# Kernel optimization log

Measured on AMD Instinct MI355X. Metric: run time of the kernel, lower is better.

## Reference

```python
import jax, jax.numpy as jnp
import numpy as np

NUM_LAYERS = 3
INPUT_SIZE = 64
EMB = 128
NUM_CAT = 128          # must equal EMB for the W_e_proj assignment to shape-check
NUM_QUERIES = 1
INIT_SCALE = 0.02
KERNEL_PARAM = 1.0     # referenced-but-undefined in source; standard alpha=1
B = 16
N = 2048
D = INPUT_SIZE + 2 * EMB                 # 320, transformer embedding dim
F_IN = INPUT_SIZE + NUM_CAT + EMB        # 320, raw input feature dim


def setup_inputs() -> dict:
    key = jax.random.key(0)
    k = jax.random.split(key, 6)
    x = jax.random.normal(k[0], (B, F_IN, N), dtype=jnp.float32)
    embedding_matrix = jax.random.normal(k[1], (EMB, NUM_CAT), dtype=jnp.float32)
    W_Q = jax.random.normal(k[2], (NUM_LAYERS, 1, D, D), dtype=jnp.float32) * INIT_SCALE
    W_K = jax.random.normal(k[3], (NUM_LAYERS, 1, D, D), dtype=jnp.float32) * INIT_SCALE
    W_V = jax.random.normal(k[4], (NUM_LAYERS, 1, D, D), dtype=jnp.float32) * INIT_SCALE
    P = jax.random.normal(k[5], (NUM_LAYERS, 1, D, D), dtype=jnp.float32) * INIT_SCALE
    return {"x": x, "embedding_matrix": embedding_matrix,
            "W_Q": W_Q, "W_K": W_K, "W_V": W_V, "P": P}


def _build_We(embedding_matrix):
    W = jnp.zeros((D, F_IN), dtype=embedding_matrix.dtype)
    W = W.at[:INPUT_SIZE, :INPUT_SIZE].set(jnp.eye(INPUT_SIZE, dtype=W.dtype))
    W = W.at[D - EMB:, F_IN - EMB:].set(jnp.eye(EMB, dtype=W.dtype))
    # rows [input_size : D-emb], cols [input_size : F-num_categories]
    W = W.at[INPUT_SIZE:D - EMB, INPUT_SIZE:F_IN - NUM_CAT].set(embedding_matrix)
    return W


def reference(x, embedding_matrix, W_Q, W_K, W_V, P):
    W = _build_We(embedding_matrix)
    h = jnp.einsum('df,bfn->bdn', W, x)                        # [B, D, N]
    for nl in range(NUM_LAYERS):
        key = h[:, :, :-NUM_QUERIES]                           # include_query=False
        value = key
        query = h
        n_context = key.shape[-1]
        Q = jnp.einsum('id,bdm->bim', W_Q[nl, 0], query)       # [B, D, N]
        K = jnp.einsum('id,bdn->bin', W_K[nl, 0], key)         # [B, D, M]
        V = jnp.einsum('id,bdn->bin', W_V[nl, 0], value)       # [B, D, M]
        # linear kernel scores
        scores = KERNEL_PARAM * jnp.einsum('bim,bin->bmn', Q, K)  # [B, N, M]
        attn = jnp.einsum('bin,bmn->bim', V, scores) / n_context  # [B, D, N]
        h = h + jnp.einsum('ji,bim->bjm', P[nl, 0], attn)
    f = h[:, -EMB:, :]                                         # [B, EMB, N] (squeeze no-op for B>1)
    logits = jnp.einsum('bdn,dc->bnc', f, embedding_matrix)    # [B, N, C]
    predictions = jax.nn.softmax(logits, axis=-1)
    return logits, predictions
```

## Files before the change

kernel.cpp:

```cpp
#include <hip/hip_runtime.h>
#include <math.h>

typedef long long ll;
typedef unsigned int uint;
typedef unsigned short ushort;
typedef __attribute__((ext_vector_type(4))) float f32x4;
typedef __attribute__((ext_vector_type(8))) short bf16x8;

#define SZ 102400LL
#define RS 40960LL

__device__ inline void split2(float v, ushort& h, ushort& l)
{
    uint u = __float_as_uint(v);
    uint uh = u + (0x7FFFu + ((u >> 16) & 1u));
    h = (ushort)(uh >> 16);
    float hf = __uint_as_float((uint)h << 16);
    float d = v - hf;
    uint ud = __float_as_uint(d);
    l = (ushort)((ud + (0x7FFFu + ((ud >> 16) & 1u))) >> 16);
}
__device__ inline float us2f(ushort h, ushort l)
{
    return __uint_as_float((uint)h << 16) + __uint_as_float((uint)l << 16);
}

__global__ __launch_bounds__(256) void gram_sp_k(
    const float* __restrict__ x, float* __restrict__ part,
    const float* __restrict__ Wq, const float* __restrict__ Wk,
    const float* __restrict__ Wv, const float* __restrict__ P,
    const float* __restrict__ emb,
    ushort* __restrict__ WqTs, ushort* __restrict__ WkTs, ushort* __restrict__ WvTs,
    ushort* __restrict__ Ps, ushort* __restrict__ embs, ushort* __restrict__ embTs,
    float* __restrict__ q0)
{
    __shared__ __align__(16) char smem[20480];
    int bid0 = blockIdx.x, tid = threadIdx.x;
    if (bid0 < 960) {
        ushort* Ah  = (ushort*)smem;
        ushort* Al_ = Ah + 2560;
        ushort* Bh  = Al_ + 2560;
        ushort* Bl_ = Bh + 2560;
        int flat = bid0;
        int swz = (flat & 7) * 120 + (flat >> 3);
        int b = swz / 60;
        int rr = swz - b * 60;
        int p = rr / 15, t = rr - p * 15;
        int ti = 0, rem = t;
        while (rem >= 5 - ti) { rem -= 5 - ti; ++ti; }
        int tj = ti + rem;
        int i0 = ti * 64, j0 = tj * 64;
        bool diag = (ti == tj);
        const float* X = x + (ll)b * 320 * 2048;
        int wv = tid >> 6, lane = tid & 63;
        int lr = lane & 15, kb = (lane >> 4) * 8;
        int cr = tid >> 2, ck = (tid & 3) * 8;
        f32x4 hh[4], hl[4], lh[4];
        f32x4 zz = {0.f, 0.f, 0.f, 0.f};
        #pragma unroll
        for (int f = 0; f < 4; ++f) { hh[f] = zz; hl[f] = zz; lh[f] = zz; }
        const ushort* BhS = diag ? Ah : Bh;
        const ushort* BlS = diag ? Al_ : Bl_;

        for (int it = 0; it < 16; ++it) {
            int kg0 = p * 512 + it * 32;
            {
                const float* src = X + (ll)(i0 + cr) * 2048 + kg0 + ck;
                float4 v0 = *(const float4*)src;
                float4 v1 = *(const float4*)(src + 4);
                float vals[8] = {v0.x,v0.y,v0.z,v0.w,v1.x,v1.y,v1.z,v1.w};
                if (kg0 + ck + 7 >= 2047) {
                    #pragma unroll
                    for (int u = 0; u < 8; ++u) if (kg0 + ck + u >= 2047) vals[u] = 0.f;
                }
                bf16x8 hv, lv;
                #pragma unroll
                for (int u = 0; u < 8; ++u) { ushort h, l; split2(vals[u], h, l);
                                              hv[u] = (short)h; lv[u] = (short)l; }
                *(bf16x8*)&Ah[cr * 40 + ck] = hv;
                *(bf16x8*)&Al_[cr * 40 + ck] = lv;
            }
            if (!diag) {
                const float* src = X + (ll)(j0 + cr) * 2048 + kg0 + ck;
                float4 v0 = *(const float4*)src;
                float4 v1 = *(const float4*)(src + 4);
                float vals[8] = {v0.x,v0.y,v0.z,v0.w,v1.x,v1.y,v1.z,v1.w};
                if (kg0 + ck + 7 >= 2047) {
                    #pragma unroll
                    for (int u = 0; u < 8; ++u) if (kg0 + ck + u >= 2047) vals[u] = 0.f;
                }
                bf16x8 hv, lv;
                #pragma unroll
                for (int u = 0; u < 8; ++u) { ushort h, l; split2(vals[u], h, l);
                                              hv[u] = (short)h; lv[u] = (short)l; }
                *(bf16x8*)&Bh[cr * 40 + ck] = hv;
                *(bf16x8*)&Bl_[cr * 40 + ck] = lv;
            }
            __syncthreads();
            bf16x8 ah = *(const bf16x8*)&Ah[(wv * 16 + lr) * 40 + kb];
            bf16x8 al = *(const bf16x8*)&Al_[(wv * 16 + lr) * 40 + kb];
            #pragma unroll
            for (int f = 0; f < 4; ++f) {
                bf16x8 bh_ = *(const bf16x8*)&BhS[(f * 16 + lr) * 40 + kb];
                bf16x8 bl_ = *(const bf16x8*)&BlS[(f * 16 + lr) * 40 + kb];
                hh[f] = __builtin_amdgcn_mfma_f32_16x16x32_bf16(ah, bh_, hh[f], 0, 0, 0);
                hl[f] = __builtin_amdgcn_mfma_f32_16x16x32_bf16(ah, bl_, hl[f], 0, 0, 0);
                lh[f] = __builtin_amdgcn_mfma_f32_16x16x32_bf16(al, bh_, lh[f], 0, 0, 0);
            }
            __syncthreads();
        }
        float* out = part + (((ll)p * 16 + b) * 15 + t) * 4096;
        int orow0 = wv * 16 + (lane >> 4) * 4;
        #pragma unroll
        for (int f = 0; f < 4; ++f) {
            int col = f * 16 + lr;
            #pragma unroll
            for (int r = 0; r < 4; ++r)
                out[(orow0 + r) * 64 + col] = hh[f][r] + hl[f][r] + lh[f][r];
        }
        return;
    }
    int bid = bid0 - 960;
    float (*T)[65] = (float(*)[65])smem;
    if (bid < 225) {
        int m = bid / 25, t = bid % 25;
        const float* mats[3] = {Wq, Wk, Wv};
        ushort* dsts[3] = {WqTs, WkTs, WvTs};
        const float* src = mats[m / 3] + (ll)(m % 3) * SZ;
        ushort* dst = dsts[m / 3] + (ll)(m % 3) * SZ;
        int r0 = (t / 5) * 64, c0 = (t % 5) * 64;
        #pragma unroll
        for (int s = 0; s < 4; ++s) {
            int idx = s * 256 + tid;
            int r = idx >> 4, cq = (idx & 15) * 4;
            *(float4*)&T[r][cq] = *(const float4*)(src + (ll)(r0 + r) * 320 + c0 + cq);
        }
        __syncthreads();
        {
            int c = tid >> 2, kq = (tid & 3) * 16;
            bf16x8 h0, h1, l0, l1;
            #pragma unroll
            for (int u = 0; u < 8; ++u) {
                ushort h, l;
                split2(T[kq + u][c], h, l);     h0[u] = (short)h; l0[u] = (short)l;
                split2(T[kq + 8 + u][c], h, l); h1[u] = (short)h; l1[u] = (short)l;
            }
            ushort* dh = dst + (ll)(c0 + c) * 320 + r0 + kq;
            *(bf16x8*)dh = h0; *(bf16x8*)(dh + 8) = h1;
            *(bf16x8*)(dh + 3 * SZ) = l0; *(bf16x8*)(dh + 3 * SZ + 8) = l1;
        }
    } else if (bid < 375) {
        ll off = (ll)(bid - 225) * 2048 + tid * 8;
        float4 v0 = *(const float4*)(P + off);
        float4 v1 = *(const float4*)(P + off + 4);
        float vals[8] = {v0.x,v0.y,v0.z,v0.w,v1.x,v1.y,v1.z,v1.w};
        bf16x8 hv, lv;
        #pragma unroll
        for (int u = 0; u < 8; ++u) { ushort h,l; split2(vals[u],h,l);
                                      hv[u]=(short)h; lv[u]=(short)l; }
        *(bf16x8*)(Ps + off) = hv;
        *(bf16x8*)(Ps + off + 3 * SZ) = lv;
    } else if (bid < 383) {
        ll off = (ll)(bid - 375) * 2048 + tid * 8;
        float4 v0 = *(const float4*)(emb + off);
        float4 v1 = *(const float4*)(emb + off + 4);
        float vals[8] = {v0.x,v0.y,v0.z,v0.w,v1.x,v1.y,v1.z,v1.w};
        bf16x8 hv, lv;
        #pragma unroll
        for (int u = 0; u < 8; ++u) { ushort h,l; split2(vals[u],h,l);
                                      hv[u]=(short)h; lv[u]=(short)l; }
        *(bf16x8*)(embs + off) = hv;
        *(bf16x8*)(embs + off + 16384) = lv;
    } else if (bid < 387) {
        int t = bid - 383;
        int r0 = (t >> 1) * 64, c0 = (t & 1) * 64;
        {
            int r = tid >> 2, cq = (tid & 3) * 4;
            *(float4*)&T[r][cq]      = *(const float4*)(emb + (ll)(r0 + r) * 128 + c0 + cq);
            *(float4*)&T[r][cq + 16] = *(const float4*)(emb + (ll)(r0 + r) * 128 + c0 + cq + 16);
            *(float4*)&T[r][cq + 32] = *(const float4*)(emb + (ll)(r0 + r) * 128 + c0 + cq + 32);
            *(float4*)&T[r][cq + 48] = *(const float4*)(emb + (ll)(r0 + r) * 128 + c0 + cq + 48);
        }
        __syncthreads();
        {
            int c = tid >> 2, kq = (tid & 3) * 16;
            bf16x8 h0, h1, l0, l1;
            #pragma unroll
            for (int u = 0; u < 8; ++u) {
                ushort h, l;
                split2(T[kq + u][c], h, l);     h0[u]=(short)h; l0[u]=(short)l;
                split2(T[kq + 8 + u][c], h, l); h1[u]=(short)h; l1[u]=(short)l;
            }
            ushort* dh = embTs + (ll)(c0 + c) * 128 + r0 + kq;
            *(bf16x8*)dh = h0; *(bf16x8*)(dh + 8) = h1;
            *(bf16x8*)(dh + 16384) = l0; *(bf16x8*)(dh + 16384 + 8) = l1;
        }
    } else {
        ll base = (ll)(bid - 387) * 2048;
        #pragma unroll
        for (int s = 0; s < 8; ++s) {
            ll id = base + s * 256 + tid;
            int c = (int)(id / 320), i = (int)(id % 320);
            q0[id] = (i >= 192) ? emb[(ll)(i - 192) * 128 + c] : 0.f;
        }
    }
}

__global__ __launch_bounds__(256) void gram_red_k(const float* __restrict__ part,
                                                  ushort* __restrict__ GxS,
                                                  ushort* __restrict__ T1s)
{
    int bt = blockIdx.x;
    int b = bt / 15, t = bt % 15;
    int ti = 0, rem = t;
    while (rem >= 5 - ti) { rem -= 5 - ti; ++ti; }
    int tj = ti + rem;
    int i0 = ti * 64, j0 = tj * 64;
    int tid = threadIdx.x;
    int tx = tid & 15, rg = tid >> 4;
    bool wi = (ti == 0 || ti >= 3);
    bool wj = (tj == 0 || tj >= 3);
    ushort* Gb = GxS + (ll)b * SZ;
    ushort* Tsb = T1s + (ll)b * SZ;
    #pragma unroll
    for (int m = 0; m < 4; ++m) {
        int r = rg * 4 + m;
        float s[4] = {};
        for (int p = 0; p < 4; ++p) {
            const float* src = part + (((ll)p * 16 + b) * 15 + t) * 4096 + r * 64 + tx * 4;
            float4 v = *(const float4*)src;
            s[0]+=v.x; s[1]+=v.y; s[2]+=v.z; s[3]+=v.w;
        }
        #pragma unroll
        for (int u = 0; u < 4; ++u) {
            ushort h, l; split2(s[u], h, l);
            ll rd = (ll)(i0 + r) * 320 + j0 + tx * 4 + u;
            ll rt = (ll)(j0 + tx * 4 + u) * 320 + (i0 + r);
            Gb[rd] = h; Gb[rd + 16 * SZ] = l;
            Gb[rt] = h; Gb[rt + 16 * SZ] = l;
            if (wi) { Tsb[rd] = h; Tsb[rd + 16 * SZ] = l; }
            if (wj) { Tsb[rt] = h; Tsb[rt + 16 * SZ] = l; }
        }
    }
}

struct CJob {
    const ushort *Ah, *Bh;
    const void *Ci, *Ci2;
    float* C; ushort* Cs;
    ll aB, bB, ciB, ci2B, cB, csB;
    ll aLo, bLo, csLo, ciLo, ci2Lo;
    int aS, bS, ciS, ci2S, cS, csS;
    int K, tN, tpb, flags;
    int swzQ, swzR;
    float alpha;
};
struct CPack { CJob j[4]; };

__global__ __launch_bounds__(256) void mchain_k(CPack jp, int c0, int c1, int c2)
{
    int bid = blockIdx.x;
    int ji, local;
    if (bid < c0)      { ji = 0; local = bid; }
    else if (bid < c1) { ji = 1; local = bid - c0; }
    else if (bid < c2) { ji = 2; local = bid - c1; }
    else               { ji = 3; local = bid - c2; }
    CJob j = jp.j[ji];
    int xcd = local & 7, sidx = local >> 3;
    int base = (xcd < j.swzR) ? xcd * (j.swzQ + 1)
                              : j.swzR * (j.swzQ + 1) + (xcd - j.swzR) * j.swzQ;
    int swz = base + sidx;
    int bz = swz / j.tpb;
    int t = swz - bz * j.tpb;
    int i0 = (t / j.tN) * 64, j0 = (t % j.tN) * 64;
    int tid = threadIdx.x;
    int wv = tid >> 6, lane = tid & 63;
    int lr = lane & 15, kb = (lane >> 4) * 8;
    f32x4 hh[4], cx[4];
    f32x4 zz = {0.f,0.f,0.f,0.f};
    #pragma unroll
    for (int f = 0; f < 4; ++f) { hh[f] = zz; cx[f] = zz; }

    __shared__ __align__(16) ushort Bsh[2][2][2560];

    if (j.K > 0) {
        int srow = tid >> 2, skq = (tid & 3) * 8;
        const ushort* Bg = j.Bh + (ll)bz * j.bB + (ll)(j0 + srow) * j.bS + skq;
        const ushort* Ar = j.Ah + (ll)bz * j.aB + (ll)(i0 + wv * 16 + lr) * j.aS + kb;
        bf16x8 svh, svl, ah, al, ahn, aln;
        svh = *(const bf16x8*)Bg;
        svl = *(const bf16x8*)(Bg + j.bLo);
        *(bf16x8*)&Bsh[0][0][srow * 40 + skq] = svh;
        *(bf16x8*)&Bsh[0][1][srow * 40 + skq] = svl;
        ah = *(const bf16x8*)Ar;
        al = *(const bf16x8*)(Ar + j.aLo);
        __syncthreads();
        int nit = j.K >> 5;
        for (int it = 0; it < nit; ++it) {
            int cur = it & 1;
            bool more = (it + 1 < nit);
            if (more) {
                int k1 = (it + 1) << 5;
                svh = *(const bf16x8*)(Bg + k1);
                svl = *(const bf16x8*)(Bg + j.bLo + k1);
                ahn = *(const bf16x8*)(Ar + k1);
                aln = *(const bf16x8*)(Ar + j.aLo + k1);
            }
            #pragma unroll
            for (int f = 0; f < 4; ++f) {
                bf16x8 bh = *(const bf16x8*)&Bsh[cur][0][(f * 16 + lr) * 40 + kb];
                bf16x8 bl = *(const bf16x8*)&Bsh[cur][1][(f * 16 + lr) * 40 + kb];
                hh[f] = __builtin_amdgcn_mfma_f32_16x16x32_bf16(ah, bh, hh[f], 0, 0, 0);
                cx[f] = __builtin_amdgcn_mfma_f32_16x16x32_bf16(ah, bl, cx[f], 0, 0, 0);
                cx[f] = __builtin_amdgcn_mfma_f32_16x16x32_bf16(al, bh, cx[f], 0, 0, 0);
            }
            if (more) {
                *(bf16x8*)&Bsh[cur ^ 1][0][srow * 40 + skq] = svh;
                *(bf16x8*)&Bsh[cur ^ 1][1][srow * 40 + skq] = svl;
                ah = ahn; al = aln;
            }
            __syncthreads();
        }
    }
    const float* Cif = (const float*)j.Ci;
    const ushort* Ciu = (const ushort*)j.Ci;
    const float* Ci2f = (const float*)j.Ci2;
    const ushort* Ci2u = (const ushort*)j.Ci2;
    float* Cp = j.C + (ll)bz * j.cB;
    ushort* Csp = j.Cs + (ll)bz * j.csB;
    int r0 = i0 + wv * 16 + ((lane >> 4) << 2);
    #pragma unroll
    for (int f = 0; f < 4; ++f) {
        int col = j0 + f * 16 + lr;
        #pragma unroll
        for (int r = 0; r < 4; ++r) {
            int row = r0 + r;
            float v = j.alpha * (hh[f][r] + cx[f][r]);
            if (j.flags & 1)
                v += Cif[(ll)bz * j.ciB + (ll)row * j.ciS + col];
            if (j.flags & 32) {
                const ushort* p = Ciu + (ll)bz * j.ciB + (ll)row * j.ciS + col;
                v += us2f(p[0], p[j.ciLo]);
            }
            if (j.flags & 64) {
                const ushort* b2 = Ci2u + (ll)bz * j.ci2B;
                if (j.flags & 2) { const ushort* p = b2 + (ll)row * j.ci2S + col;
                                   v += us2f(p[0], p[j.ci2Lo]); }
                if (j.flags & 4) { const ushort* p = b2 + (ll)col * j.ci2S + row;
                                   v += us2f(p[0], p[j.ci2Lo]); }
            } else {
                if (j.flags & 2) v += Ci2f[(ll)bz * j.ci2B + (ll)row * j.ci2S + col];
                if (j.flags & 4) v += Ci2f[(ll)bz * j.ci2B + (ll)col * j.ci2S + row];
            }
            if (j.flags & 8) Cp[(ll)row * j.cS + col] = v;
            if (j.flags & 16) {
                ushort h, l; split2(v, h, l);
                ushort* p = Csp + (ll)row * j.csS + col;
                p[0] = h; p[j.csLo] = l;
            }
        }
    }
}

__global__ __launch_bounds__(256) void logits_mfma_k(const float* __restrict__ x,
                                                     const ushort* __restrict__ LBs,
                                                     float* __restrict__ logits,
                                                     float* __restrict__ pred)
{
    int flat = blockIdx.x;
    int swzb = (flat & 7) * 128 + (flat >> 3);
    int b = swzb >> 6;
    int i0 = (swzb & 63) * 32;
    const float* X = x + (ll)b * 320 * 2048;
    const ushort* LB = LBs + (ll)b * RS;
    __shared__ float Xs_[2][32][33];
    __shared__ float pmL[2][32], psL[2][32];
    int tid = threadIdx.x;
    int wv = tid >> 6, lane = tid & 63;
    int lr = lane & 15, g = lane >> 4, kb = g * 8;
    int rowg = (wv & 1) * 16, ch = wv >> 1, colh = ch * 64;
    int lkk = tid >> 3, lq = (tid & 7) * 4;
    f32x4 hh[4], cx[4];
    f32x4 zz = {0.f,0.f,0.f,0.f};
    #pragma unroll
    for (int f = 0; f < 4; ++f) { hh[f] = zz; cx[f] = zz; }
    float4 pa;
    auto glb = [&](int k0) {
        pa = *(const float4*)(X + (ll)(k0 + lkk) * 2048 + i0 + lq);
    };
    auto stl = [&](int buf) {
        float* p = &Xs_[buf][lkk][lq];
        p[0] = pa.x; p[1] = pa.y; p[2] = pa.z; p[3] = pa.w;
    };
    glb(0); stl(0);
    __syncthreads();
    for (int it = 0; it < 10; ++it) {
        int cur = it & 1;
        if (it < 9) glb((it + 1) * 32);
        bf16x8 ah, al;
        #pragma unroll
        for (int u = 0; u < 8; ++u) {
            ushort h, l;
            split2(Xs_[cur][kb + u][rowg + lr], h, l);
            ah[u] = (short)h; al[u] = (short)l;
        }
        #pragma unroll
        for (int f = 0; f < 4; ++f) {
            const ushort* Bp = LB + (ll)(colh + f * 16 + lr) * 320 + it * 32 + kb;
            bf16x8 bh = *(const bf16x8*)Bp;
            bf16x8 bl = *(const bf16x8*)(Bp + 16 * RS);
            hh[f] = __builtin_amdgcn_mfma_f32_16x16x32_bf16(ah, bh, hh[f], 0, 0, 0);
            cx[f] = __builtin_amdgcn_mfma_f32_16x16x32_bf16(ah, bl, cx[f], 0, 0, 0);
            cx[f] = __builtin_amdgcn_mfma_f32_16x16x32_bf16(al, bh, cx[f], 0, 0, 0);
        }
        if (it < 9) stl(cur ^ 1);
        __syncthreads();
    }
    float v[4][4];
    #pragma unroll
    for (int r = 0; r < 4; ++r)
        #pragma unroll
        for (int f = 0; f < 4; ++f) v[r][f] = hh[f][r] + cx[f][r];
    #pragma unroll
    for (int r = 0; r < 4; ++r) {
        float m = fmaxf(fmaxf(v[r][0], v[r][1]), fmaxf(v[r][2], v[r][3]));
        #pragma unroll
        for (int off = 8; off; off >>= 1) m = fmaxf(m, __shfl_xor(m, off));
        if (lr == 0) pmL[ch][rowg + g * 4 + r] = m;
    }
    __syncthreads();
    float ev[4][4];
    #pragma unroll
    for (int r = 0; r < 4; ++r) {
        int blr = rowg + g * 4 + r;
        float mx = fmaxf(pmL[0][blr], pmL[1][blr]);
        float s = 0.f;
        #pragma unroll
        for (int f = 0; f < 4; ++f) { ev[r][f] = expf(v[r][f] - mx); s += ev[r][f]; }
        #pragma unroll
        for (int off = 8; off; off >>= 1) s += __shfl_xor(s, off);
        if (lr == 0) psL[ch][blr] = s;
    }
    __syncthreads();
    #pragma unroll
    for (int r = 0; r < 4; ++r) {
        int blr = rowg + g * 4 + r;
        float inv = 1.f / (psL[0][blr] + psL[1][blr]);
        ll ro = ((ll)b * 2048 + i0 + blr) * 128 + colh + lr;
        #pragma unroll
        for (int f = 0; f < 4; ++f) {
            logits[ro + f * 16] = v[r][f];
            pred[ro + f * 16] = ev[r][f] * inv;
        }
    }
}

extern "C" void kernel_launch(void* const* d_in, const int* in_sizes, int n_in,
                              void* d_out, int out_size, void* d_ws, size_t ws_size,
                              hipStream_t stream)
{
    const float* x   = (const float*)d_in[0];
    const float* emb = (const float*)d_in[1];
    const float* Wq  = (const float*)d_in[2];
    const float* Wk  = (const float*)d_in[3];
    const float* Wv  = (const float*)d_in[4];
    const float* P   = (const float*)d_in[5];

    float* logits = (float*)d_out;
    float* pred   = logits + (ll)16 * 2048 * 128;

    float* w = (float*)d_ws;
    auto takef = [&](ll n) { float* p = w; w += n; return p; };
    ushort* GxS  = (ushort*)takef(16 * SZ);
    ushort* T1s  = (ushort*)takef(16 * SZ);
    ushort* Gs   = (ushort*)takef(16 * SZ);
    ushort* As   = (ushort*)takef(16 * SZ);
    ushort* Us   = (ushort*)takef(16 * SZ);
    float*  ATsF = takef(48 * SZ);
    ushort* ATs  = (ushort*)ATsF;
    ushort* PVs  = (ushort*)takef(3 * SZ);
    ushort* KQTs = (ushort*)takef(3 * SZ);
    ushort* KQs  = (ushort*)takef(3 * SZ);
    ushort* Ps   = (ushort*)takef(3 * SZ);
    ushort* WqTs = (ushort*)takef(3 * SZ);
    ushort* WkTs = (ushort*)takef(3 * SZ);
    ushort* WvTs = (ushort*)takef(3 * SZ);
    ushort* embs = (ushort*)takef(16384);
    ushort* embTs= (ushort*)takef(16384);
    float*  q0f  = takef(RS);
    ushort* q1s  = (ushort*)takef(16 * RS);
    ushort* q2s  = (ushort*)takef(16 * RS);
    ushort* LBs  = (ushort*)takef(16 * RS);
    ushort* Xs   = GxS;
    ushort* Zts  = T1s;
    float*  part = ATsF;
    ushort* q3s  = q1s;
    const float cinv = 1.f / 2047.f;

    auto JB = [](const ushort* Ah, ll aB, int aS, ll aLo,
                 const ushort* Bh, ll bB, int bS, ll bLo,
                 int K, int tM, int tN, float alpha, int flags,
                 const void* Ci, ll ciB, int ciS, ll ciLo,
                 const void* Ci2, ll ci2B, int ci2S, ll ci2Lo,
                 float* C, ll cB, int cS,
                 ushort* Cs, ll csB, int csS, ll csLo) {
        CJob j;
        j.Ah = Ah; j.Bh = Bh;
        j.Ci = Ci; j.Ci2 = Ci2; j.C = C; j.Cs = Cs;
        j.aB = aB; j.bB = bB; j.ciB = ciB; j.ci2B = ci2B; j.cB = cB; j.csB = csB;
        j.aLo = aLo; j.bLo = bLo; j.csLo = csLo; j.ciLo = ciLo; j.ci2Lo = ci2Lo;
        j.aS = aS; j.bS = bS; j.ciS = ciS; j.ci2S = ci2S; j.cS = cS; j.csS = csS;
        j.K = K; j.tN = tN; j.tpb = tM * tN; j.flags = flags; j.alpha = alpha;
        j.swzQ = 0; j.swzR = 0;
        return j;
    };
    auto fire = [&](const CJob* js, const int* nb, int n) {
        CPack jp;
        int cum[4], tot = 0;
        for (int i = 0; i < 4; ++i) {
            jp.j[i] = js[i < n ? i : 0];
            if (i < n) { jp.j[i].swzQ = nb[i] >> 3; jp.j[i].swzR = nb[i] & 7; }
            tot += (i < n ? nb[i] : 0);
            cum[i] = tot;
        }
        mchain_k<<<tot, 256, 0, stream>>>(jp, cum[0], cum[1], cum[2]);
    };

    gram_sp_k<<<1367, 256, 0, stream>>>(x, part, Wq, Wk, Wv, P, emb,
                                        WqTs, WkTs, WvTs, Ps, embs, embTs, q0f);
    gram_red_k<<<240, 256, 0, stream>>>(part, GxS, T1s);
    {
        CJob js[4] = {
            JB(embs, 0, 128, 16384,  GxS + 64, SZ, 320, 16*SZ,  128, 2, 5, 1.f, 16,
               0,0,0,0, 0,0,0,0,  0,0,0,  T1s + 64*320, SZ, 320, 16*SZ),
            JB(Ps, SZ, 320, 3*SZ,  WvTs, SZ, 320, 3*SZ,  320, 5, 5, 1.f, 16,
               0,0,0,0, 0,0,0,0,  0,0,0,  PVs, SZ, 320, 3*SZ),
            JB(WqTs, SZ, 320, 3*SZ,  WkTs, SZ, 320, 3*SZ,  320, 5, 5, 1.f, 16,
               0,0,0,0, 0,0,0,0,  0,0,0,  KQTs, SZ, 320, 3*SZ),
            JB(WkTs, SZ, 320, 3*SZ,  WqTs, SZ, 320, 3*SZ,  320, 5, 5, 1.f, 16,
               0,0,0,0, 0,0,0,0,  0,0,0,  KQs, SZ, 320, 3*SZ)};
        int nb[4] = {160, 75, 75, 75};
        fire(js, nb, 4);
    }
    {
        CJob js[3] = {
            JB(T1s + 64, SZ, 320, 16*SZ,  embs, 0, 128, 16384,  128, 5, 2, 1.f, 16,
               0,0,0,0, 0,0,0,0,  0,0,0,  Gs + 64, SZ, 320, 16*SZ),
            JB(0,0,0,0, 0,0,0,0,  0, 5, 1, 0.f, 32|16,
               T1s, SZ, 320, 16*SZ, 0,0,0,0,  0,0,0,  Gs, SZ, 320, 16*SZ),
            JB(0,0,0,0, 0,0,0,0,  0, 5, 2, 0.f, 32|16,
               T1s + 192, SZ, 320, 16*SZ, 0,0,0,0,  0,0,0,  Gs + 192, SZ, 320, 16*SZ)};
        int nb[3] = {160, 80, 160};
        fire(js, nb, 3);
    }
    for (int l = 0; l < 3; ++l) {
        const ushort* PVl = PVs + (ll)l * SZ;
        const ushort* KQTl = KQTs + (ll)l * SZ;
        const ushort* KQl = KQs + (ll)l * SZ;
        ushort* ATl = ATs + (ll)l * 16 * SZ;
        if (l < 2) {
            CJob s1[2] = {
                JB(PVl, 0, 320, 3*SZ,  Gs, SZ, 320, 16*SZ,  320, 5, 5, 1.f, 16,
                   0,0,0,0, 0,0,0,0,  0,0,0,  Xs, SZ, 320, 16*SZ),
                JB(Gs, SZ, 320, 16*SZ,  KQl, 0, 320, 3*SZ,  320, 5, 5, 1.f, 16,
                   0,0,0,0, 0,0,0,0,  0,0,0,  Zts, SZ, 320, 16*SZ)};
            int n1[2] = {400, 400};
            fire(s1, n1, 2);
            CJob s2[3] = {
                JB(Xs, SZ, 320, 16*SZ,  KQTl, 0, 320, 3*SZ,  320, 5, 5, cinv, 16,
                   0,0,0,0, 0,0,0,0,  0,0,0,  As, SZ, 320, 16*SZ),
                JB(KQTl, 0, 320, 3*SZ,  Xs, SZ, 320, 16*SZ,  320, 5, 5, cinv, 16,
                   0,0,0,0, 0,0,0,0,  0,0,0,  ATl, SZ, 320, 48*SZ),
                JB(Xs, SZ, 320, 16*SZ,  Zts, SZ, 320, 16*SZ,  320, 5, 5, cinv, 16,
                   0,0,0,0, 0,0,0,0,  0,0,0,  Us, SZ, 320, 16*SZ)};
            int n2[3] = {400, 400, 400};
            fire(s2, n2, 3);
            CJob s3[1] = {
                JB(Us, SZ, 320, 16*SZ,  As, SZ, 320, 16*SZ,  320, 5, 5, 1.f, 16|32|2|4|64,
                   Gs, SZ, 320, 16*SZ,  Us, SZ, 320, 16*SZ,  0,0,0,  Gs, SZ, 320, 16*SZ)};
            int n3[1] = {400};
            fire(s3, n3, 1);
        } else {
            CJob s1[1] = {
                JB(PVl, 0, 320, 3*SZ,  Gs, SZ, 320, 16*SZ,  320, 5, 5, 1.f, 16,
                   0,0,0,0, 0,0,0,0,  0,0,0,  Xs, SZ, 320, 16*SZ)};
            int n1[1] = {400};
            fire(s1, n1, 1);
            CJob s2[1] = {
                JB(KQTl, 0, 320, 3*SZ,  Xs, SZ, 320, 16*SZ,  320, 5, 5, cinv, 16,
                   0,0,0,0, 0,0,0,0,  0,0,0,  ATl, SZ, 320, 48*SZ)};
            int n2[1] = {400};
            fire(s2, n2, 1);
        }
    }
    {
        CJob js[1] = {
            JB(embTs, 0, 128, 16384,  ATs + 2*16*SZ + 192, SZ, 320, 48*SZ,  128, 2, 5, 1.f, 1|16,
               q0f, 0, 320, 0, 0,0,0,0,  0,0,0,  q1s, RS, 320, 16*RS)};
        int nb[1] = {160};
        fire(js, nb, 1);
    }
    {
        CJob js[1] = {
            JB(q1s, RS, 320, 16*RS,  ATs + 1*16*SZ, SZ, 320, 48*SZ,  320, 2, 5, 1.f, 32|16,
               q1s, RS, 320, 16*RS, 0,0,0,0,  0,0,0,  q2s, RS, 320, 16*RS)};
        int nb[1] = {160};
        fire(js, nb, 1);
    }
    {
        CJob js[1] = {
            JB(q2s, RS, 320, 16*RS,  ATs, SZ, 320, 48*SZ,  320, 2, 5, 1.f, 32|16,
               q2s, RS, 320, 16*RS, 0,0,0,0,  0,0,0,  q3s, RS, 320, 16*RS)};
        int nb[1] = {160};
        fire(js, nb, 1);
    }
    {
        CJob js[3] = {
            JB(q3s + 64, RS, 320, 16*RS,  embTs, 0, 128, 16384,  128, 2, 2, 1.f, 16,
               0,0,0,0, 0,0,0,0,  0,0,0,  LBs + 64, RS, 320, 16*RS),
            JB(0,0,0,0, 0,0,0,0,  0, 2, 1, 0.f, 32|16,
               q3s, RS, 320, 16*RS, 0,0,0,0,  0,0,0,  LBs, RS, 320, 16*RS),
            JB(0,0,0,0, 0,0,0,0,  0, 2, 2, 0.f, 32|16,
               q3s + 192, RS, 320, 16*RS, 0,0,0,0,  0,0,0,  LBs + 192, RS, 320, 16*RS)};
        int nb[3] = {64, 32, 64};
        fire(js, nb, 3);
    }
    logits_mfma_k<<<1024, 256, 0, stream>>>(x, LBs, logits, pred);
}
```

Before: 315.4 us.

## Fuse q-chain GEMM launches into one kernel and coalesce logits stores

Replaces the four generic job launches that propagate the query-side product through the three layers and into LBs with one dedicated kernel. Each block keeps its 32-column slice of q in shared memory as split bf16 hi/lo and applies the three layer updates plus the embedding projection in place. This removes three launches and the q1/q2 intermediate round trips through global memory. It also hoists the B-operand loads in the logits kernel ahead of the split and stages logits and predictions through shared memory for float4 coalesced stores. The cost is that the fused kernel runs only 64 blocks, which limits parallelism, and the logits kernel gains extra shared memory and barriers.

```diff
diff --git a/kernel.cpp b/kernel.cpp
--- a/kernel.cpp
+++ b/kernel.cpp
@@ -362,6 +362,139 @@
     }
 }
 
+__global__ __launch_bounds__(256) void qchain_k(const float* __restrict__ q0f,
+                                                const ushort* __restrict__ ATs,
+                                                const ushort* __restrict__ embTs,
+                                                ushort* __restrict__ LBs)
+{
+    __shared__ __align__(16) ushort qh[32][328], ql[32][328];
+    int bid = blockIdx.x, tid = threadIdx.x;
+    int swz = (bid & 7) * 8 + (bid >> 3);
+    int b = swz >> 2, cs = swz & 3;
+    int c0 = cs * 32;
+    int wv = tid >> 6, lane = tid & 63;
+    int lr = lane & 15, g = lane >> 4, kb = g * 8;
+
+    {
+        int c = tid >> 3, iq = (tid & 7) * 40;
+        const float* src = q0f + (ll)(c0 + c) * 320 + iq;
+        #pragma unroll
+        for (int u = 0; u < 10; ++u) {
+            float4 v = *(const float4*)(src + u * 4);
+            float vals[4] = {v.x, v.y, v.z, v.w};
+            #pragma unroll
+            for (int e = 0; e < 4; ++e) {
+                ushort h, l; split2(vals[e], h, l);
+                qh[c][iq + u * 4 + e] = h;
+                ql[c][iq + u * 4 + e] = l;
+            }
+        }
+    }
+    __syncthreads();
+
+    for (int l = 2; l >= 0; --l) {
+        const ushort* A = ATs + ((ll)l * 16 + b) * SZ;
+        int ks0 = (l == 2) ? 6 : 0;
+        f32x4 hh[5][2], cx[5][2];
+        f32x4 zz = {0.f,0.f,0.f,0.f};
+        #pragma unroll
+        for (int t = 0; t < 5; ++t) { hh[t][0]=zz; hh[t][1]=zz; cx[t][0]=zz; cx[t][1]=zz; }
+        for (int ks = ks0; ks < 10; ++ks) {
+            int k0 = ks * 32;
+            bf16x8 ah[5], al[5];
+            #pragma unroll
+            for (int t = 0; t < 5; ++t) {
+                const ushort* Ar = A + (ll)(wv * 80 + t * 16 + lr) * 320 + k0 + kb;
+                ah[t] = *(const bf16x8*)Ar;
+                al[t] = *(const bf16x8*)(Ar + 48 * SZ);
+            }
+            bf16x8 bh[2], bl[2];
+            #pragma unroll
+            for (int ct = 0; ct < 2; ++ct) {
+                bh[ct] = *(const bf16x8*)&qh[ct * 16 + lr][k0 + kb];
+                bl[ct] = *(const bf16x8*)&ql[ct * 16 + lr][k0 + kb];
+            }
+            #pragma unroll
+            for (int t = 0; t < 5; ++t)
+                #pragma unroll
+                for (int ct = 0; ct < 2; ++ct) {
+                    hh[t][ct] = __builtin_amdgcn_mfma_f32_16x16x32_bf16(ah[t], bh[ct], hh[t][ct], 0, 0, 0);
+                    cx[t][ct] = __builtin_amdgcn_mfma_f32_16x16x32_bf16(ah[t], bl[ct], cx[t][ct], 0, 0, 0);
+                    cx[t][ct] = __builtin_amdgcn_mfma_f32_16x16x32_bf16(al[t], bh[ct], cx[t][ct], 0, 0, 0);
+                }
+        }
+        __syncthreads();
+        #pragma unroll
+        for (int t = 0; t < 5; ++t)
+            #pragma unroll
+            for (int ct = 0; ct < 2; ++ct)
+                #pragma unroll
+                for (int r = 0; r < 4; ++r) {
+                    int i = wv * 80 + t * 16 + g * 4 + r;
+                    int c = ct * 16 + lr;
+                    float v = us2f(qh[c][i], ql[c][i]) + hh[t][ct][r] + cx[t][ct][r];
+                    ushort h, l2; split2(v, h, l2);
+                    qh[c][i] = h; ql[c][i] = l2;
+                }
+        __syncthreads();
+    }
+
+    ushort* LBb = LBs + (ll)b * RS;
+    {
+        #pragma unroll
+        for (int s = 0; s < 3; ++s) {
+            int t = s * 256 + tid;
+            int c = t / 24, u = t % 24;
+            int f0 = (u < 8) ? u * 8 : 192 + (u - 8) * 8;
+            *(bf16x8*)(LBb + (ll)(c0 + c) * 320 + f0) = *(const bf16x8*)&qh[c][f0];
+            *(bf16x8*)(LBb + 16 * RS + (ll)(c0 + c) * 320 + f0) = *(const bf16x8*)&ql[c][f0];
+        }
+    }
+    {
+        f32x4 mh[2][2], mc[2][2];
+        f32x4 zz = {0.f,0.f,0.f,0.f};
+        #pragma unroll
+        for (int t = 0; t < 2; ++t) { mh[t][0]=zz; mh[t][1]=zz; mc[t][0]=zz; mc[t][1]=zz; }
+        for (int ks = 0; ks < 4; ++ks) {
+            int k0 = ks * 32;
+            bf16x8 eh[2], el[2];
+            #pragma unroll
+            for (int tu = 0; tu < 2; ++tu) {
+                const ushort* Er = embTs + (ll)(wv * 32 + tu * 16 + lr) * 128 + k0 + kb;
+                eh[tu] = *(const bf16x8*)Er;
+                el[tu] = *(const bf16x8*)(Er + 16384);
+            }
+            bf16x8 bh[2], bl[2];
+            #pragma unroll
+            for (int ct = 0; ct < 2; ++ct) {
+                bh[ct] = *(const bf16x8*)&qh[ct * 16 + lr][64 + k0 + kb];
+                bl[ct] = *(const bf16x8*)&ql[ct * 16 + lr][64 + k0 + kb];
+            }
+            #pragma unroll
+            for (int tu = 0; tu < 2; ++tu)
+                #pragma unroll
+                for (int ct = 0; ct < 2; ++ct) {
+                    mh[tu][ct] = __builtin_amdgcn_mfma_f32_16x16x32_bf16(eh[tu], bh[ct], mh[tu][ct], 0, 0, 0);
+                    mc[tu][ct] = __builtin_amdgcn_mfma_f32_16x16x32_bf16(eh[tu], bl[ct], mc[tu][ct], 0, 0, 0);
+                    mc[tu][ct] = __builtin_amdgcn_mfma_f32_16x16x32_bf16(el[tu], bh[ct], mc[tu][ct], 0, 0, 0);
+                }
+        }
+        #pragma unroll
+        for (int tu = 0; tu < 2; ++tu)
+            #pragma unroll
+            for (int ct = 0; ct < 2; ++ct)
+                #pragma unroll
+                for (int r = 0; r < 4; ++r) {
+                    int u = wv * 32 + tu * 16 + g * 4 + r;
+                    int c = ct * 16 + lr;
+                    float v = mh[tu][ct][r] + mc[tu][ct][r];
+                    ushort h, l2; split2(v, h, l2);
+                    ll o = (ll)(c0 + c) * 320 + 64 + u;
+                    LBb[o] = h; LBb[o + 16 * RS] = l2;
+                }
+    }
+}
+
 __global__ __launch_bounds__(256) void logits_mfma_k(const float* __restrict__ x,
                                                      const ushort* __restrict__ LBs,
                                                      float* __restrict__ logits,
@@ -374,6 +507,7 @@
     const float* X = x + (ll)b * 320 * 2048;
     const ushort* LB = LBs + (ll)b * RS;
     __shared__ float Xs_[2][32][33];
+    __shared__ float SB[32][132];
     __shared__ float pmL[2][32], psL[2][32];
     int tid = threadIdx.x;
     int wv = tid >> 6, lane = tid & 63;
@@ -397,6 +531,15 @@
     for (int it = 0; it < 10; ++it) {
         int cur = it & 1;
         if (it < 9) glb((it + 1) * 32);
+        const ushort* B0 = LB + (ll)(colh + lr) * 320 + it * 32 + kb;
+        bf16x8 b0h = *(const bf16x8*)B0;
+        bf16x8 b0l = *(const bf16x8*)(B0 + 16 * RS);
+        bf16x8 b1h = *(const bf16x8*)(B0 + 16 * 320);
+        bf16x8 b1l = *(const bf16x8*)(B0 + 16 * 320 + 16 * RS);
+        bf16x8 b2h = *(const bf16x8*)(B0 + 32 * 320);
+        bf16x8 b2l = *(const bf16x8*)(B0 + 32 * 320 + 16 * RS);
+        bf16x8 b3h = *(const bf16x8*)(B0 + 48 * 320);
+        bf16x8 b3l = *(const bf16x8*)(B0 + 48 * 320 + 16 * RS);
         bf16x8 ah, al;
         #pragma unroll
         for (int u = 0; u < 8; ++u) {
@@ -404,15 +547,18 @@
             split2(Xs_[cur][kb + u][rowg + lr], h, l);
             ah[u] = (short)h; al[u] = (short)l;
         }
-        #pragma unroll
-        for (int f = 0; f < 4; ++f) {
-            const ushort* Bp = LB + (ll)(colh + f * 16 + lr) * 320 + it * 32 + kb;
-            bf16x8 bh = *(const bf16x8*)Bp;
-            bf16x8 bl = *(const bf16x8*)(Bp + 16 * RS);
-            hh[f] = __builtin_amdgcn_mfma_f32_16x16x32_bf16(ah, bh, hh[f], 0, 0, 0);
-            cx[f] = __builtin_amdgcn_mfma_f32_16x16x32_bf16(ah, bl, cx[f], 0, 0, 0);
-            cx[f] = __builtin_amdgcn_mfma_f32_16x16x32_bf16(al, bh, cx[f], 0, 0, 0);
-        }
+        hh[0] = __builtin_amdgcn_mfma_f32_16x16x32_bf16(ah, b0h, hh[0], 0, 0, 0);
+        cx[0] = __builtin_amdgcn_mfma_f32_16x16x32_bf16(ah, b0l, cx[0], 0, 0, 0);
+        cx[0] = __builtin_amdgcn_mfma_f32_16x16x32_bf16(al, b0h, cx[0], 0, 0, 0);
+        hh[1] = __builtin_amdgcn_mfma_f32_16x16x32_bf16(ah, b1h, hh[1], 0, 0, 0);
+        cx[1] = __builtin_amdgcn_mfma_f32_16x16x32_bf16(ah, b1l, cx[1], 0, 0, 0);
+        cx[1] = __builtin_amdgcn_mfma_f32_16x16x32_bf16(al, b1h, cx[1], 0, 0, 0);
+        hh[2] = __builtin_amdgcn_mfma_f32_16x16x32_bf16(ah, b2h, hh[2], 0, 0, 0);
+        cx[2] = __builtin_amdgcn_mfma_f32_16x16x32_bf16(ah, b2l, cx[2], 0, 0, 0);
+        cx[2] = __builtin_amdgcn_mfma_f32_16x16x32_bf16(al, b2h, cx[2], 0, 0, 0);
+        hh[3] = __builtin_amdgcn_mfma_f32_16x16x32_bf16(ah, b3h, hh[3], 0, 0, 0);
+        cx[3] = __builtin_amdgcn_mfma_f32_16x16x32_bf16(ah, b3l, cx[3], 0, 0, 0);
+        cx[3] = __builtin_amdgcn_mfma_f32_16x16x32_bf16(al, b3h, cx[3], 0, 0, 0);
         if (it < 9) stl(cur ^ 1);
         __syncthreads();
     }
@@ -429,7 +575,7 @@
         if (lr == 0) pmL[ch][rowg + g * 4 + r] = m;
     }
     __syncthreads();
-    float ev[4][4];
+    float ev[4][4], inv[4];
     #pragma unroll
     for (int r = 0; r < 4; ++r) {
         int blr = rowg + g * 4 + r;
@@ -445,13 +591,32 @@
     #pragma unroll
     for (int r = 0; r < 4; ++r) {
         int blr = rowg + g * 4 + r;
-        float inv = 1.f / (psL[0][blr] + psL[1][blr]);
-        ll ro = ((ll)b * 2048 + i0 + blr) * 128 + colh + lr;
-        #pragma unroll
-        for (int f = 0; f < 4; ++f) {
-            logits[ro + f * 16] = v[r][f];
-            pred[ro + f * 16] = ev[r][f] * inv;
-        }
+        inv[r] = 1.f / (psL[0][blr] + psL[1][blr]);
+    }
+    #pragma unroll
+    for (int r = 0; r < 4; ++r)
+        #pragma unroll
+        for (int f = 0; f < 4; ++f)
+            SB[rowg + g * 4 + r][colh + f * 16 + lr] = v[r][f];
+    __syncthreads();
+    #pragma unroll
+    for (int s = 0; s < 4; ++s) {
+        int idx = s * 256 + tid;
+        int row = idx >> 5, cq = (idx & 31) * 4;
+        *(float4*)(logits + ((ll)b * 2048 + i0 + row) * 128 + cq) = *(float4*)&SB[row][cq];
+    }
+    __syncthreads();
+    #pragma unroll
+    for (int r = 0; r < 4; ++r)
+        #pragma unroll
+        for (int f = 0; f < 4; ++f)
+            SB[rowg + g * 4 + r][colh + f * 16 + lr] = ev[r][f] * inv[r];
+    __syncthreads();
+    #pragma unroll
+    for (int s = 0; s < 4; ++s) {
+        int idx = s * 256 + tid;
+        int row = idx >> 5, cq = (idx & 31) * 4;
+        *(float4*)(pred + ((ll)b * 2048 + i0 + row) * 128 + cq) = *(float4*)&SB[row][cq];
     }
 }
 
@@ -488,13 +653,10 @@
     ushort* embs = (ushort*)takef(16384);
     ushort* embTs= (ushort*)takef(16384);
     float*  q0f  = takef(RS);
-    ushort* q1s  = (ushort*)takef(16 * RS);
-    ushort* q2s  = (ushort*)takef(16 * RS);
     ushort* LBs  = (ushort*)takef(16 * RS);
     ushort* Xs   = GxS;
     ushort* Zts  = T1s;
     float*  part = ATsF;
-    ushort* q3s  = q1s;
     const float cinv = 1.f / 2047.f;
 
     auto JB = [](const ushort* Ah, ll aB, int aS, ll aLo,
@@ -593,37 +755,6 @@
             fire(s2, n2, 1);
         }
     }
-    {
-        CJob js[1] = {
-            JB(embTs, 0, 128, 16384,  ATs + 2*16*SZ + 192, SZ, 320, 48*SZ,  128, 2, 5, 1.f, 1|16,
-               q0f, 0, 320, 0, 0,0,0,0,  0,0,0,  q1s, RS, 320, 16*RS)};
-        int nb[1] = {160};
-        fire(js, nb, 1);
-    }
-    {
-        CJob js[1] = {
-            JB(q1s, RS, 320, 16*RS,  ATs + 1*16*SZ, SZ, 320, 48*SZ,  320, 2, 5, 1.f, 32|16,
-               q1s, RS, 320, 16*RS, 0,0,0,0,  0,0,0,  q2s, RS, 320, 16*RS)};
-        int nb[1] = {160};
-        fire(js, nb, 1);
-    }
-    {
-        CJob js[1] = {
-            JB(q2s, RS, 320, 16*RS,  ATs, SZ, 320, 48*SZ,  320, 2, 5, 1.f, 32|16,
-               q2s, RS, 320, 16*RS, 0,0,0,0,  0,0,0,  q3s, RS, 320, 16*RS)};
-        int nb[1] = {160};
-        fire(js, nb, 1);
-    }
-    {
-        CJob js[3] = {
-            JB(q3s + 64, RS, 320, 16*RS,  embTs, 0, 128, 16384,  128, 2, 2, 1.f, 16,
-               0,0,0,0, 0,0,0,0,  0,0,0,  LBs + 64, RS, 320, 16*RS),
-            JB(0,0,0,0, 0,0,0,0,  0, 2, 1, 0.f, 32|16,
-               q3s, RS, 320, 16*RS, 0,0,0,0,  0,0,0,  LBs, RS, 320, 16*RS),
-            JB(0,0,0,0, 0,0,0,0,  0, 2, 2, 0.f, 32|16,
-               q3s + 192, RS, 320, 16*RS, 0,0,0,0,  0,0,0,  LBs + 192, RS, 320, 16*RS)};
-        int nb[3] = {64, 32, 64};
-        fire(js, nb, 3);
-    }
+    qchain_k<<<64, 256, 0, stream>>>(q0f, ATs, embTs, LBs);
     logits_mfma_k<<<1024, 256, 0, stream>>>(x, LBs, logits, pred);
 }
```

New measurement: 323.1 us. +2.4%, slower.
